# Kernel tuning notes

Hardware: AMD Instinct MI355X
Metric: run time of the kernel (lower is better)

## Reference

```python
import jax, jax.numpy as jnp
import numpy as np

E = 1024   # embed_dim
H = 16     # num_heads
D = E // H # head dim = 64
NUM_BUCKETS = 32
MAX_DISTANCE = 128


def _relative_position_bucket(rel, num_buckets=NUM_BUCKETS, max_distance=MAX_DISTANCE):
    # T5-style bucketing (bidirectional): sign half + log-spaced far buckets.
    nb = num_buckets // 2
    buckets = (rel > 0).astype(jnp.int32) * nb
    rel = jnp.abs(rel)
    max_exact = nb // 2
    is_small = rel < max_exact
    # clamp to >=1 before log to avoid -inf on the masked-out branch
    rel_f = jnp.maximum(rel, 1).astype(jnp.float32)
    large = max_exact + (
        jnp.log(rel_f / max_exact) / np.log(max_distance / max_exact) * (nb - max_exact)
    ).astype(jnp.int32)
    large = jnp.minimum(large, nb - 1)
    return buckets + jnp.where(is_small, rel, large)


def setup_inputs() -> dict:
    key = jax.random.key(0)
    ks = jax.random.split(key, 6)
    B, S, K = 2, 2048, 2048
    w = 0.02
    return {
        "hidden_states": jax.random.normal(ks[0], (B, S, E), jnp.float32),
        "key_value_states": jax.random.normal(ks[1], (B, K, E), jnp.float32),
        "Wq": jax.random.normal(ks[2], (E, E), jnp.float32) * w,
        "Wkv": jax.random.normal(ks[3], (E, 2 * E), jnp.float32) * w,
        "Wo": jax.random.normal(ks[4], (E, E), jnp.float32) * w,
        "rel_bias": jax.random.normal(ks[5], (NUM_BUCKETS, H), jnp.float32) * w,
    }


def reference(hidden_states, key_value_states, Wq, Wkv, Wo, rel_bias):
    B, S, _ = hidden_states.shape
    K = key_value_states.shape[1]
    # projections (no bias, no 1/sqrt(d) scaling — T5 style)
    q = (hidden_states @ Wq).reshape(B, S, H, D).transpose(0, 2, 1, 3)      # [B,H,S,D]
    kv = (key_value_states @ Wkv).reshape(B, K, 2, H, D)
    k = kv[:, :, 0].transpose(0, 2, 1, 3)                                   # [B,H,K,D]
    v = kv[:, :, 1].transpose(0, 2, 1, 3)                                   # [B,H,K,D]
    scores = jnp.einsum('bhsd,bhkd->bhsk', q, k)                            # [B,H,S,K]
    # relative position bias
    rel = jnp.arange(K)[None, :] - jnp.arange(S)[:, None]                   # [S,K]
    buckets = _relative_position_bucket(rel)                                # [S,K]
    bias = rel_bias[buckets].transpose(2, 0, 1)[None]                       # [1,H,S,K]
    scores = scores + bias
    attn = jax.nn.softmax(scores.astype(jnp.float32), axis=-1).astype(scores.dtype)
    out = jnp.einsum('bhsk,bhkd->bshd', attn, v).reshape(B, S, E)
    return out @ Wo
```

## Files before the change

### kernel.cpp

```cpp
#include <hip/hip_runtime.h>
#include <hip/hip_bf16.h>
#include <math.h>

typedef __hip_bfloat16 bf16;
typedef __bf16 bf16x4 __attribute__((ext_vector_type(4)));
typedef __bf16 bf16x8 __attribute__((ext_vector_type(8)));
typedef float f32x4 __attribute__((ext_vector_type(4)));
typedef float f32x16 __attribute__((ext_vector_type(16)));
typedef unsigned short us4 __attribute__((ext_vector_type(4)));

#define LOG2E 1.44269504088896340736f

#if defined(__has_builtin)
#if __has_builtin(__builtin_amdgcn_exp2f)
#define EXP2(x) __builtin_amdgcn_exp2f(x)
#else
#define EXP2(x) exp2f(x)
#endif
#else
#define EXP2(x) exp2f(x)
#endif

__device__ inline __bf16 f2b(float f) {
  __hip_bfloat16 h = __float2bfloat16(f);
  return *reinterpret_cast<__bf16*>(&h);
}
__device__ inline unsigned short b2u(float f) {
  __hip_bfloat16 h = __float2bfloat16(f);
  return *reinterpret_cast<unsigned short*>(&h);
}
__device__ inline unsigned pk2(float a, float b) {
  __hip_bfloat162 t = __float22bfloat162_rn(make_float2(a, b));
  return *reinterpret_cast<unsigned*>(&t);
}
__device__ inline bf16x8 ld16(const bf16* p) {
  bf16x4 lo = *(const bf16x4*)p;
  bf16x4 hi = *(const bf16x4*)(p + 4);
  return __builtin_shufflevector(lo, hi, 0, 1, 2, 3, 4, 5, 6, 7);
}
__device__ inline void st16(bf16* p, uint4 v) {
  *(uint2*)p = make_uint2(v.x, v.y);
  *(uint2*)(p + 4) = make_uint2(v.z, v.w);
}
__device__ inline us4 shfl32_us4(us4 v) {
  uint2 u = *(uint2*)&v;
  u.x = __shfl_xor(u.x, 32);
  u.y = __shfl_xor(u.y, 32);
  return *(us4*)&u;
}
__device__ inline bf16x8 mk8(us4 lo, us4 hi) {
  bf16x4 l = *(bf16x4*)&lo;
  bf16x4 h = *(bf16x4*)&hi;
  return __builtin_shufflevector(l, h, 0, 1, 2, 3, 4, 5, 6, 7);
}
__device__ inline void async16(const bf16* g, bf16* l) {
  __builtin_amdgcn_global_load_lds(
      (const __attribute__((address_space(1))) unsigned int*)g,
      (__attribute__((address_space(3))) unsigned int*)l, 16, 0, 0);
}

__global__ void cast2_k(const float* __restrict__ a, const float* __restrict__ b,
                        bf16* __restrict__ oa, bf16* __restrict__ ob) {
  int gid = blockIdx.x * 256 + threadIdx.x;
  const float* in = (gid < 524288) ? a : b;
  bf16* out = (gid < 524288) ? oa : ob;
  int i = (gid & 524287) * 8;
  float4 a0 = *(const float4*)(in + i);
  float4 a1 = *(const float4*)(in + i + 4);
  bf16x8 v;
  v[0] = f2b(a0.x); v[1] = f2b(a0.y); v[2] = f2b(a0.z); v[3] = f2b(a0.w);
  v[4] = f2b(a1.x); v[5] = f2b(a1.y); v[6] = f2b(a1.z); v[7] = f2b(a1.w);
  *(bf16x8*)(out + i) = v;
}

__global__ void transpose_all_k(const float* __restrict__ Wq, const float* __restrict__ Wkv,
                                const float* __restrict__ Wo, bf16* __restrict__ WqT,
                                bf16* __restrict__ WkvT, bf16* __restrict__ WoT) {
  __shared__ float tile[32][33];
  int z = blockIdx.z;
  const float* in = z == 0 ? Wq : (z == 1 ? Wkv : Wo);
  bf16* out = z == 0 ? WqT : (z == 1 ? WkvT : WoT);
  int cols = z == 1 ? 2048 : 1024;
  int c0 = blockIdx.x * 32;
  if (c0 >= cols) return;
  int r0 = blockIdx.y * 32;
  int tx = threadIdx.x, ty = threadIdx.y;
  for (int i = ty; i < 32; i += 8)
    tile[i][tx] = in[(size_t)(r0 + i) * cols + c0 + tx];
  __syncthreads();
  for (int i = ty; i < 32; i += 8)
    out[(size_t)(c0 + i) * 1024 + r0 + tx] = __float2bfloat16(tile[tx][i]);
}

__global__ void bias_lut_k(const float* __restrict__ rel_bias, float* __restrict__ lut) {
  int r = blockIdx.x * blockDim.x + threadIdx.x;
  if (r >= 4096) return;
  int rel = r - 2048;
  int b = rel > 0 ? 16 : 0;
  int ar = rel < 0 ? -rel : rel;
  int idx;
  if (ar < 8) {
    idx = b + ar;
  } else {
    double t = log((double)ar / 8.0) / log(16.0) * 8.0;
    int lg = 8 + (int)t;
    if (lg > 15) lg = 15;
    idx = b + lg;
  }
  for (int h = 0; h < 16; ++h)
    lut[h * 4096 + r] = rel_bias[idx * 16 + h] * LOG2E;
}

__global__ __launch_bounds__(256) void gemm_qkv_k(const bf16* __restrict__ hbf,
                                                  const bf16* __restrict__ kbf,
                                                  const bf16* __restrict__ WqT,
                                                  const bf16* __restrict__ WkvT,
                                                  bf16* __restrict__ Qb,
                                                  bf16* __restrict__ Kb,
                                                  bf16* __restrict__ Vt) {
  __shared__ __align__(16) bf16 As[128 * 64];
  __shared__ __align__(16) bf16 Bs[128 * 64];
  const int tid = threadIdx.x;
  const int lane = tid & 63;
  const int w = tid >> 6;
  const int wm = (w >> 1) * 64;
  const int wn = (w & 1) * 64;
  const int l15 = lane & 15;
  const int quad = lane >> 4;
  const int r8 = lane >> 3;
  const int clog = (lane & 7) ^ r8;

  const bool isQ = blockIdx.y < 8;
  const bf16* A = isQ ? hbf : kbf;
  const bf16* Bt = isQ ? WqT : WkvT;
  const int n0 = (isQ ? blockIdx.y : blockIdx.y - 8) * 128;
  const int m0 = blockIdx.x * 128;
  const bool isV = (!isQ) && (n0 >= 1024);

  f32x4 acc[4][4];
#pragma unroll
  for (int i = 0; i < 4; ++i)
#pragma unroll
    for (int j = 0; j < 4; ++j) acc[i][j] = (f32x4){0.f, 0.f, 0.f, 0.f};

  for (int k0 = 0; k0 < 1024; k0 += 64) {
    __syncthreads();
#pragma unroll
    for (int rep = 0; rep < 4; ++rep) {
      int seg = w * 4 + rep;
      async16(A + (size_t)(m0 + seg * 8 + r8) * 1024 + k0 + clog * 8, As + seg * 512);
      async16(Bt + (size_t)(n0 + seg * 8 + r8) * 1024 + k0 + clog * 8, Bs + seg * 512);
    }
    __syncthreads();
#pragma unroll
    for (int kc = 0; kc < 2; ++kc) {
      bf16x8 af[4], bfr[4];
#pragma unroll
      for (int i = 0; i < 4; ++i) {
        int row = wm + i * 16 + l15;
        af[i] = *(const bf16x8*)(As + row * 64 + (((kc * 4 + quad) ^ (row & 7)) << 3));
      }
#pragma unroll
      for (int j = 0; j < 4; ++j) {
        int row = wn + j * 16 + l15;
        bfr[j] = *(const bf16x8*)(Bs + row * 64 + (((kc * 4 + quad) ^ (row & 7)) << 3));
      }
      if (isV) {
#pragma unroll
        for (int i = 0; i < 4; ++i)
#pragma unroll
          for (int j = 0; j < 4; ++j)
            acc[i][j] = __builtin_amdgcn_mfma_f32_16x16x32_bf16(af[i], bfr[j], acc[i][j], 0, 0, 0);
      } else {
#pragma unroll
        for (int i = 0; i < 4; ++i)
#pragma unroll
          for (int j = 0; j < 4; ++j)
            acc[i][j] = __builtin_amdgcn_mfma_f32_16x16x32_bf16(bfr[j], af[i], acc[i][j], 0, 0, 0);
      }
    }
  }

  if (isV) {
#pragma unroll
    for (int i = 0; i < 4; ++i) {
      int gmb = m0 + wm + i * 16 + quad * 4;
      int b = gmb >> 11, kp = gmb & 2047;
#pragma unroll
      for (int j = 0; j < 4; ++j) {
        int gn = n0 + wn + j * 16 + l15;
        int h = (gn >> 6) & 15, d = gn & 63;
        uint2 u;
        u.x = pk2(acc[i][j][0], acc[i][j][1]);
        u.y = pk2(acc[i][j][2], acc[i][j][3]);
        *(uint2*)(Vt + ((((size_t)b * 16 + h) * 64 + d) << 11) + kp) = u;
      }
    }
    return;
  }
  const float scale = isQ ? LOG2E : 1.0f;
  bf16* dst = isQ ? Qb : Kb;
#pragma unroll
  for (int i = 0; i < 4; ++i) {
    int gm = m0 + wm + i * 16 + l15;
    int b = gm >> 11, s = gm & 2047;
#pragma unroll
    for (int j = 0; j < 4; ++j) {
      int gn = n0 + wn + j * 16 + quad * 4;
      int h = (gn >> 6) & 15, d0 = gn & 63;
      uint2 u;
      u.x = pk2(acc[i][j][0] * scale, acc[i][j][1] * scale);
      u.y = pk2(acc[i][j][2] * scale, acc[i][j][3] * scale);
      *(uint2*)(dst + ((((size_t)b * 16 + h) * 2048 + s) << 6) + d0) = u;
    }
  }
}

__global__ __launch_bounds__(256) void gemm_o_k(const bf16* __restrict__ A,
                                                const bf16* __restrict__ Bt,
                                                float* __restrict__ C0) {
  __shared__ __align__(16) bf16 As[128 * 64];
  __shared__ __align__(16) bf16 Bs[64 * 64];
  const int tid = threadIdx.x;
  const int lane = tid & 63;
  const int w = tid >> 6;
  const int wm = w * 32;
  const int m0 = blockIdx.x * 128;
  const int n0 = blockIdx.y * 64;
  const int l15 = lane & 15;
  const int quad = lane >> 4;
  const int r8 = lane >> 3;
  const int clog = (lane & 7) ^ r8;

  f32x4 acc[2][4];
#pragma unroll
  for (int i = 0; i < 2; ++i)
#pragma unroll
    for (int j = 0; j < 4; ++j) acc[i][j] = (f32x4){0.f, 0.f, 0.f, 0.f};

  for (int k0 = 0; k0 < 1024; k0 += 64) {
    __syncthreads();
#pragma unroll
    for (int rep = 0; rep < 4; ++rep) {
      int seg = w * 4 + rep;
      async16(A + (size_t)(m0 + seg * 8 + r8) * 1024 + k0 + clog * 8, As + seg * 512);
    }
#pragma unroll
    for (int rep = 0; rep < 2; ++rep) {
      int seg = w * 2 + rep;
      async16(Bt + (size_t)(n0 + seg * 8 + r8) * 1024 + k0 + clog * 8, Bs + seg * 512);
    }
    __syncthreads();
#pragma unroll
    for (int kc = 0; kc < 2; ++kc) {
      bf16x8 af[2], bfr[4];
#pragma unroll
      for (int i = 0; i < 2; ++i) {
        int row = wm + i * 16 + l15;
        af[i] = *(const bf16x8*)(As + row * 64 + (((kc * 4 + quad) ^ (row & 7)) << 3));
      }
#pragma unroll
      for (int j = 0; j < 4; ++j) {
        int row = j * 16 + l15;
        bfr[j] = *(const bf16x8*)(Bs + row * 64 + (((kc * 4 + quad) ^ (row & 7)) << 3));
      }
#pragma unroll
      for (int i = 0; i < 2; ++i)
#pragma unroll
        for (int j = 0; j < 4; ++j)
          acc[i][j] = __builtin_amdgcn_mfma_f32_16x16x32_bf16(bfr[j], af[i], acc[i][j], 0, 0, 0);
    }
  }
#pragma unroll
  for (int i = 0; i < 2; ++i) {
    int gm = m0 + wm + i * 16 + l15;
#pragma unroll
    for (int j = 0; j < 4; ++j) {
      int gn = n0 + j * 16 + quad * 4;
      *(f32x4*)(C0 + (size_t)gm * 1024 + gn) = acc[i][j];
    }
  }
}

#define STK 68
#define SVK 136
__global__ __launch_bounds__(256) void attn_k(const bf16* __restrict__ Qb,
                                              const bf16* __restrict__ Kb,
                                              const bf16* __restrict__ Vt,
                                              const float* __restrict__ lut,
                                              bf16* __restrict__ Ob) {
  __shared__ float lbias[2176];
  __shared__ __align__(16) bf16 Ks[128 * STK];
  __shared__ __align__(16) bf16 Vs[64 * SVK];

  const int tid = threadIdx.x;
  const int lane = tid & 63;
  const int w = tid >> 6;
  const int q31 = lane & 31;
  const int half = lane >> 5;

  const int qt = blockIdx.x;
  const int bh = blockIdx.y;
  const int h = bh & 15, b = bh >> 4;
  const int qb = qt * 128;

  const int gbase = h * 4096 + 1921 - qb;
  for (int t = tid; t < 2175; t += 256) lbias[t] = lut[gbase + t];

  const float c_pos = lut[h * 4096 + 2048 + 120];
  const float c_neg = lut[h * 4096 + 2048 - 120];

  const size_t base = (size_t)bh * 2048 * 64;
  const size_t vbase = (size_t)bh * 64 * 2048;
  const int qg = qb + w * 32 + q31;

  bf16x8 qf[4];
#pragma unroll
  for (int c = 0; c < 4; ++c)
    qf[c] = *(const bf16x8*)(Qb + base + (size_t)qg * 64 + c * 16 + half * 8);

  f32x16 oacc[2];
#pragma unroll
  for (int dj = 0; dj < 2; ++dj)
#pragma unroll
    for (int r = 0; r < 16; ++r) oacc[dj][r] = 0.f;
  float l_run = 0.f;

  uint4 kreg[4], vreg[4];
#pragma unroll
  for (int rep = 0; rep < 4; ++rep) {
    int slot = tid + rep * 256;
    kreg[rep] = *(const uint4*)(Kb + base + (size_t)(slot >> 3) * 64 + (slot & 7) * 8);
    vreg[rep] = *(const uint4*)(Vt + vbase + (size_t)(slot >> 4) * 2048 + (slot & 15) * 8);
  }

  for (int kt = 0; kt < 2048; kt += 128) {
    __syncthreads();
#pragma unroll
    for (int rep = 0; rep < 4; ++rep) {
      int slot = tid + rep * 256;
      st16(Ks + (slot >> 3) * STK + (slot & 7) * 8, kreg[rep]);
      st16(Vs + (slot >> 4) * SVK + (slot & 15) * 8, vreg[rep]);
    }
    __syncthreads();
    if (kt + 128 < 2048) {
#pragma unroll
      for (int rep = 0; rep < 4; ++rep) {
        int slot = tid + rep * 256;
        kreg[rep] = *(const uint4*)(Kb + base + (size_t)(kt + 128 + (slot >> 3)) * 64 + (slot & 7) * 8);
        vreg[rep] = *(const uint4*)(Vt + vbase + (size_t)(slot >> 4) * 2048 + kt + 128 + (slot & 15) * 8);
      }
    }

    f32x16 sacc[4];
#pragma unroll
    for (int mt = 0; mt < 4; ++mt) {
#pragma unroll
      for (int r = 0; r < 16; ++r) sacc[mt][r] = 0.f;
#pragma unroll
      for (int c = 0; c < 4; ++c) {
        bf16x8 kf = ld16(Ks + (mt * 32 + q31) * STK + c * 16 + half * 8);
        sacc[mt] = __builtin_amdgcn_mfma_f32_32x32x16_bf16(kf, qf[c], sacc[mt], 0, 0, 0);
      }
    }

    bool farp = (kt - qg) >= 91;
    bool farn = (qg - (kt + 127)) >= 91;
    float sum0 = 0.f, sum1 = 0.f;
    if (__ballot(farp | farn) == 0xFFFFFFFFFFFFFFFFull) {
      float cb = farp ? c_pos : c_neg;
#pragma unroll
      for (int mt = 0; mt < 4; ++mt)
#pragma unroll
        for (int r = 0; r < 16; ++r) {
          float p = EXP2(sacc[mt][r] + cb);
          sacc[mt][r] = p;
          if (r & 1) sum1 += p; else sum0 += p;
        }
    } else {
      const int xbase = kt + 127 + 4 * half - w * 32 - q31;
#pragma unroll
      for (int mt = 0; mt < 4; ++mt)
#pragma unroll
        for (int g = 0; g < 4; ++g) {
          int x0 = xbase + mt * 32 + 8 * g;
#pragma unroll
          for (int rr = 0; rr < 4; ++rr) {
            float p = EXP2(sacc[mt][4 * g + rr] + lbias[x0 + rr]);
            sacc[mt][4 * g + rr] = p;
            if (rr & 1) sum1 += p; else sum0 += p;
          }
        }
    }
    float sum = sum0 + sum1;
    sum += __shfl_xor(sum, 32);
    l_run += sum;

    us4 ownq[4][4], rcv[4][2];
#pragma unroll
    for (int mt = 0; mt < 4; ++mt) {
#pragma unroll
      for (int a = 0; a < 4; ++a) {
        uint2 u;
        u.x = pk2(sacc[mt][4 * a + 0], sacc[mt][4 * a + 1]);
        u.y = pk2(sacc[mt][4 * a + 2], sacc[mt][4 * a + 3]);
        ownq[mt][a] = *(us4*)&u;
      }
      us4 s0 = half ? ownq[mt][0] : ownq[mt][1];
      us4 s1 = half ? ownq[mt][2] : ownq[mt][3];
      rcv[mt][0] = shfl32_us4(s0);
      rcv[mt][1] = shfl32_us4(s1);
    }

#pragma unroll
    for (int c = 0; c < 8; ++c) {
      int mt = c >> 1, p = c & 1;
      bf16x8 pfc = half ? mk8(rcv[mt][p], ownq[mt][2 * p + 1])
                        : mk8(ownq[mt][2 * p], rcv[mt][p]);
#pragma unroll
      for (int dj = 0; dj < 2; ++dj) {
        bf16x8 vf = ld16(Vs + (dj * 32 + q31) * SVK + c * 16 + half * 8);
        oacc[dj] = __builtin_amdgcn_mfma_f32_32x32x16_bf16(vf, pfc, oacc[dj], 0, 0, 0);
      }
    }
  }

  float inv = 1.0f / l_run;
#pragma unroll
  for (int dj = 0; dj < 2; ++dj)
#pragma unroll
    for (int g = 0; g < 4; ++g) {
      uint2 u;
      u.x = pk2(oacc[dj][4 * g + 0] * inv, oacc[dj][4 * g + 1] * inv);
      u.y = pk2(oacc[dj][4 * g + 2] * inv, oacc[dj][4 * g + 3] * inv);
      int d0 = dj * 32 + 8 * g + 4 * half;
      *(uint2*)(Ob + ((size_t)(b * 2048 + qg)) * 1024 + h * 64 + d0) = u;
    }
}

extern "C" void kernel_launch(void* const* d_in, const int* in_sizes, int n_in,
                              void* d_out, int out_size, void* d_ws, size_t ws_size,
                              hipStream_t stream) {
  const float* hidden = (const float*)d_in[0];
  const float* kvs    = (const float*)d_in[1];
  const float* Wq     = (const float*)d_in[2];
  const float* Wkv    = (const float*)d_in[3];
  const float* Wo     = (const float*)d_in[4];
  const float* relb   = (const float*)d_in[5];
  float* out = (float*)d_out;

  char* ws = (char*)d_ws;
  bf16* WqT  = (bf16*)(ws + (size_t)0);
  bf16* WkvT = (bf16*)(ws + ((size_t)2 << 20));
  bf16* WoT  = (bf16*)(ws + ((size_t)6 << 20));
  bf16* Ob   = (bf16*)(ws + ((size_t)8 << 20));
  bf16* hbf  = Ob;
  bf16* Qb   = (bf16*)(ws + ((size_t)16 << 20));
  bf16* Kb   = (bf16*)(ws + ((size_t)24 << 20));
  bf16* Vt   = (bf16*)(ws + ((size_t)32 << 20));
  float* LUT = (float*)(ws + ((size_t)40 << 20));
  bf16* kbf  = (bf16*)d_out;

  transpose_all_k<<<dim3(64, 32, 3), dim3(32, 8), 0, stream>>>(Wq, Wkv, Wo, WqT, WkvT, WoT);
  bias_lut_k<<<16, 256, 0, stream>>>(relb, LUT);
  cast2_k<<<4096, 256, 0, stream>>>(hidden, kvs, hbf, kbf);

  gemm_qkv_k<<<dim3(32, 24), 256, 0, stream>>>(hbf, kbf, WqT, WkvT, Qb, Kb, Vt);
  attn_k<<<dim3(16, 32), 256, 0, stream>>>(Qb, Kb, Vt, LUT, Ob);
  gemm_o_k<<<dim3(32, 16), 256, 0, stream>>>(Ob, WoT, out);
}
```

Before: 237.8 us.

## Merge prep kernels, store bias LUT as bf16, drop far-field fast path

The three preprocessing kernels (weight transpose, bias LUT, input cast) are folded into one launch that dispatches on block index, which removes two kernel launches and their gaps. In the attention kernel the shared-memory bias table becomes bf16, halving its footprint, and launch bounds request 4 blocks per SIMD. The far-field constant-bias branch and its ballot are removed, so every tile reads the bias table. Bias precision drops to bf16, which may change numerics slightly.

Result: slower. 353.4 us (+48.6%).

```diff
diff --git a/kernel.cpp b/kernel.cpp
--- a/kernel.cpp
+++ b/kernel.cpp
@@ -25,10 +25,6 @@
   __hip_bfloat16 h = __float2bfloat16(f);
   return *reinterpret_cast<__bf16*>(&h);
 }
-__device__ inline unsigned short b2u(float f) {
-  __hip_bfloat16 h = __float2bfloat16(f);
-  return *reinterpret_cast<unsigned short*>(&h);
-}
 __device__ inline unsigned pk2(float a, float b) {
   __hip_bfloat162 t = __float22bfloat162_rn(make_float2(a, b));
   return *reinterpret_cast<unsigned*>(&t);
@@ -59,42 +55,45 @@
       (__attribute__((address_space(3))) unsigned int*)l, 16, 0, 0);
 }
 
-__global__ void cast2_k(const float* __restrict__ a, const float* __restrict__ b,
-                        bf16* __restrict__ oa, bf16* __restrict__ ob) {
-  int gid = blockIdx.x * 256 + threadIdx.x;
-  const float* in = (gid < 524288) ? a : b;
-  bf16* out = (gid < 524288) ? oa : ob;
-  int i = (gid & 524287) * 8;
-  float4 a0 = *(const float4*)(in + i);
-  float4 a1 = *(const float4*)(in + i + 4);
-  bf16x8 v;
-  v[0] = f2b(a0.x); v[1] = f2b(a0.y); v[2] = f2b(a0.z); v[3] = f2b(a0.w);
-  v[4] = f2b(a1.x); v[5] = f2b(a1.y); v[6] = f2b(a1.z); v[7] = f2b(a1.w);
-  *(bf16x8*)(out + i) = v;
-}
-
-__global__ void transpose_all_k(const float* __restrict__ Wq, const float* __restrict__ Wkv,
-                                const float* __restrict__ Wo, bf16* __restrict__ WqT,
-                                bf16* __restrict__ WkvT, bf16* __restrict__ WoT) {
+__global__ void prep_k(const float* __restrict__ hidden, const float* __restrict__ kvs,
+                       const float* __restrict__ Wq, const float* __restrict__ Wkv,
+                       const float* __restrict__ Wo, const float* __restrict__ relb,
+                       bf16* __restrict__ hbf, bf16* __restrict__ kbf,
+                       bf16* __restrict__ WqT, bf16* __restrict__ WkvT,
+                       bf16* __restrict__ WoT, float* __restrict__ lut) {
   __shared__ float tile[32][33];
-  int z = blockIdx.z;
-  const float* in = z == 0 ? Wq : (z == 1 ? Wkv : Wo);
-  bf16* out = z == 0 ? WqT : (z == 1 ? WkvT : WoT);
-  int cols = z == 1 ? 2048 : 1024;
-  int c0 = blockIdx.x * 32;
-  if (c0 >= cols) return;
-  int r0 = blockIdx.y * 32;
-  int tx = threadIdx.x, ty = threadIdx.y;
-  for (int i = ty; i < 32; i += 8)
-    tile[i][tx] = in[(size_t)(r0 + i) * cols + c0 + tx];
-  __syncthreads();
-  for (int i = ty; i < 32; i += 8)
-    out[(size_t)(c0 + i) * 1024 + r0 + tx] = __float2bfloat16(tile[tx][i]);
-}
-
-__global__ void bias_lut_k(const float* __restrict__ rel_bias, float* __restrict__ lut) {
-  int r = blockIdx.x * blockDim.x + threadIdx.x;
-  if (r >= 4096) return;
+  const int bid = blockIdx.x;
+  const int tid = threadIdx.x;
+  if (bid < 4096) {
+    const float* in = (bid < 2048) ? hidden : kvs;
+    bf16* out = (bid < 2048) ? hbf : kbf;
+    int i = (((bid & 2047) * 256) + tid) * 8;
+    float4 a0 = *(const float4*)(in + i);
+    float4 a1 = *(const float4*)(in + i + 4);
+    bf16x8 v;
+    v[0] = f2b(a0.x); v[1] = f2b(a0.y); v[2] = f2b(a0.z); v[3] = f2b(a0.w);
+    v[4] = f2b(a1.x); v[5] = f2b(a1.y); v[6] = f2b(a1.z); v[7] = f2b(a1.w);
+    *(bf16x8*)(out + i) = v;
+    return;
+  }
+  if (bid < 8192) {
+    const float* in;
+    bf16* out;
+    int t, cols;
+    if (bid < 5120) { in = Wq; out = WqT; t = bid - 4096; cols = 1024; }
+    else if (bid < 7168) { in = Wkv; out = WkvT; t = bid - 5120; cols = 2048; }
+    else { in = Wo; out = WoT; t = bid - 7168; cols = 1024; }
+    int c0 = (cols == 2048 ? (t & 63) : (t & 31)) * 32;
+    int r0 = (cols == 2048 ? (t >> 6) : (t >> 5)) * 32;
+    int tx = tid & 31, ty = tid >> 5;
+    for (int i = ty; i < 32; i += 8)
+      tile[i][tx] = in[(size_t)(r0 + i) * cols + c0 + tx];
+    __syncthreads();
+    for (int i = ty; i < 32; i += 8)
+      out[(size_t)(c0 + i) * 1024 + r0 + tx] = __float2bfloat16(tile[tx][i]);
+    return;
+  }
+  int r = (bid - 8192) * 256 + tid;
   int rel = r - 2048;
   int b = rel > 0 ? 16 : 0;
   int ar = rel < 0 ? -rel : rel;
@@ -108,7 +107,7 @@
     idx = b + lg;
   }
   for (int h = 0; h < 16; ++h)
-    lut[h * 4096 + r] = rel_bias[idx * 16 + h] * LOG2E;
+    lut[h * 4096 + r] = relb[idx * 16 + h] * LOG2E;
 }
 
 __global__ __launch_bounds__(256) void gemm_qkv_k(const bf16* __restrict__ hbf,
@@ -284,12 +283,12 @@
 
 #define STK 68
 #define SVK 136
-__global__ __launch_bounds__(256) void attn_k(const bf16* __restrict__ Qb,
-                                              const bf16* __restrict__ Kb,
-                                              const bf16* __restrict__ Vt,
-                                              const float* __restrict__ lut,
-                                              bf16* __restrict__ Ob) {
-  __shared__ float lbias[2176];
+__global__ __launch_bounds__(256, 4) void attn_k(const bf16* __restrict__ Qb,
+                                                 const bf16* __restrict__ Kb,
+                                                 const bf16* __restrict__ Vt,
+                                                 const float* __restrict__ lut,
+                                                 bf16* __restrict__ Ob) {
+  __shared__ bf16 lbias[2176];
   __shared__ __align__(16) bf16 Ks[128 * STK];
   __shared__ __align__(16) bf16 Vs[64 * SVK];
 
@@ -305,10 +304,7 @@
   const int qb = qt * 128;
 
   const int gbase = h * 4096 + 1921 - qb;
-  for (int t = tid; t < 2175; t += 256) lbias[t] = lut[gbase + t];
-
-  const float c_pos = lut[h * 4096 + 2048 + 120];
-  const float c_neg = lut[h * 4096 + 2048 - 120];
+  for (int t = tid; t < 2175; t += 256) lbias[t] = __float2bfloat16(lut[gbase + t]);
 
   const size_t base = (size_t)bh * 2048 * 64;
   const size_t vbase = (size_t)bh * 64 * 2048;
@@ -364,34 +360,20 @@
       }
     }
 
-    bool farp = (kt - qg) >= 91;
-    bool farn = (qg - (kt + 127)) >= 91;
+    const int xbase = kt + 127 + 4 * half - w * 32 - q31;
     float sum0 = 0.f, sum1 = 0.f;
-    if (__ballot(farp | farn) == 0xFFFFFFFFFFFFFFFFull) {
-      float cb = farp ? c_pos : c_neg;
-#pragma unroll
-      for (int mt = 0; mt < 4; ++mt)
-#pragma unroll
-        for (int r = 0; r < 16; ++r) {
-          float p = EXP2(sacc[mt][r] + cb);
-          sacc[mt][r] = p;
-          if (r & 1) sum1 += p; else sum0 += p;
+#pragma unroll
+    for (int mt = 0; mt < 4; ++mt)
+#pragma unroll
+      for (int g = 0; g < 4; ++g) {
+        int x0 = xbase + mt * 32 + 8 * g;
+#pragma unroll
+        for (int rr = 0; rr < 4; ++rr) {
+          float p = EXP2(sacc[mt][4 * g + rr] + __bfloat162float(lbias[x0 + rr]));
+          sacc[mt][4 * g + rr] = p;
+          if (rr & 1) sum1 += p; else sum0 += p;
         }
-    } else {
-      const int xbase = kt + 127 + 4 * half - w * 32 - q31;
-#pragma unroll
-      for (int mt = 0; mt < 4; ++mt)
-#pragma unroll
-        for (int g = 0; g < 4; ++g) {
-          int x0 = xbase + mt * 32 + 8 * g;
-#pragma unroll
-          for (int rr = 0; rr < 4; ++rr) {
-            float p = EXP2(sacc[mt][4 * g + rr] + lbias[x0 + rr]);
-            sacc[mt][4 * g + rr] = p;
-            if (rr & 1) sum1 += p; else sum0 += p;
-          }
-        }
-    }
+      }
     float sum = sum0 + sum1;
     sum += __shfl_xor(sum, 32);
     l_run += sum;
@@ -461,10 +443,8 @@
   float* LUT = (float*)(ws + ((size_t)40 << 20));
   bf16* kbf  = (bf16*)d_out;
 
-  transpose_all_k<<<dim3(64, 32, 3), dim3(32, 8), 0, stream>>>(Wq, Wkv, Wo, WqT, WkvT, WoT);
-  bias_lut_k<<<16, 256, 0, stream>>>(relb, LUT);
-  cast2_k<<<4096, 256, 0, stream>>>(hidden, kvs, hbf, kbf);
-
+  prep_k<<<8208, 256, 0, stream>>>(hidden, kvs, Wq, Wkv, Wo, relb,
+                                   hbf, kbf, WqT, WkvT, WoT, LUT);
   gemm_qkv_k<<<dim3(32, 24), 256, 0, stream>>>(hbf, kbf, WqT, WkvT, Qb, Kb, Vt);
   attn_k<<<dim3(16, 32), 256, 0, stream>>>(Qb, Kb, Vt, LUT, Ob);
   gemm_o_k<<<dim3(32, 16), 256, 0, stream>>>(Ob, WoT, out);
```
